# Optimization experiments

Hardware: AMD Instinct MI355X
Metric: run time of the kernel (lower is better)

Reference implementation:

```python
import jax, jax.numpy as jnp
import numpy as np

L, H, D, HS, DFF, V, B, T = 4, 16, 1024, 64, 5120, 32000, 2, 1024
EPS = 1e-5


def setup_inputs() -> dict:
    key = jax.random.key(0)
    ks = iter(jax.random.split(key, 40))
    def nrm(shape):
        return jax.random.normal(next(ks), shape, dtype=jnp.float32) * 0.02
    inp = {}
    inp['idx'] = jax.random.randint(next(ks), (B, T), 0, V)
    inp['tok_emb'] = nrm((V, D))
    inp['pos_emb'] = nrm((T, D))
    for s in ('u', 'm'):  # u = unmasked heads, m = masked (causal) heads
        inp['Wq_' + s] = nrm((L, H, D, HS)); inp['bq_' + s] = jnp.zeros((L, H, HS), jnp.float32)
        inp['Wk_' + s] = nrm((L, H, D, HS)); inp['bk_' + s] = jnp.zeros((L, H, HS), jnp.float32)
        inp['Wv_' + s] = nrm((L, H, D, HS)); inp['bv_' + s] = jnp.zeros((L, H, HS), jnp.float32)
        inp['Wp_' + s] = nrm((L, D, D));     inp['bp_' + s] = jnp.zeros((L, D), jnp.float32)
    inp['W1'] = nrm((L, D, DFF)); inp['b1'] = jnp.zeros((L, DFF), jnp.float32)
    inp['W2'] = nrm((L, DFF, D)); inp['b2'] = jnp.zeros((L, D), jnp.float32)
    ones = jnp.ones((L, D), jnp.float32); zer = jnp.zeros((L, D), jnp.float32)
    inp['lnf_g'] = ones; inp['lnf_b'] = zer     # LayerNorm inside FeedForward
    inp['n1_g'] = ones;  inp['n1_b'] = zer      # Block.norm1
    inp['n2_g'] = ones;  inp['n2_b'] = zer      # Block.norm2
    inp['nf_g'] = jnp.ones((D,), jnp.float32); inp['nf_b'] = jnp.zeros((D,), jnp.float32)
    inp['Wfin'] = nrm((D, V)); inp['bfin'] = jnp.zeros((V,), jnp.float32)
    return inp


def _ln(x, g, b):
    mu = jnp.mean(x, -1, keepdims=True)
    var = jnp.mean((x - mu) ** 2, -1, keepdims=True)
    return (x - mu) / jnp.sqrt(var + EPS) * g + b


def _attn(xn, Wq, bq, Wk, bk, Wv, bv, Wp, bp, causal):
    # xn: [B,T,D]; Wq/Wk/Wv: [H,D,HS] (all heads batched in one einsum)
    q = jnp.einsum('btd,hde->bhte', xn, Wq) + bq[:, None, :]
    k = jnp.einsum('btd,hde->bhte', xn, Wk) + bk[:, None, :]
    v = jnp.einsum('btd,hde->bhte', xn, Wv) + bv[:, None, :]
    w = jnp.einsum('bhte,bhse->bhts', q, k) * (HS ** -0.5)
    if causal:
        mask = jnp.tril(jnp.ones((w.shape[-2], w.shape[-1]), bool))
        w = jnp.where(mask, w, -jnp.inf)
    w = jax.nn.softmax(w, axis=-1)
    o = jnp.einsum('bhts,bhse->bhte', w, v)
    o = o.transpose(0, 2, 1, 3).reshape(xn.shape[0], xn.shape[1], -1)  # concat heads
    return o @ Wp + bp


def _ffn(x, W1, b1, W2, b2, g, b):
    h = jax.nn.leaky_relu(x @ W1 + b1, negative_slope=0.01)
    return _ln(h @ W2 + b2, g, b)


def reference(idx, tok_emb, pos_emb,
              Wq_u, bq_u, Wk_u, bk_u, Wv_u, bv_u, Wp_u, bp_u,
              Wq_m, bq_m, Wk_m, bk_m, Wv_m, bv_m, Wp_m, bp_m,
              W1, b1, W2, b2, lnf_g, lnf_b, n1_g, n1_b, n2_g, n2_b,
              nf_g, nf_b, Wfin, bfin):
    Tn = idx.shape[1]
    x = tok_emb[idx] + pos_emb[:Tn]
    for l in range(L):
        # exact quirky Block wiring from the original code
        x2 = x + _attn(_ln(x, n1_g[l], n1_b[l]), Wq_u[l], bq_u[l], Wk_u[l], bk_u[l],
                       Wv_u[l], bv_u[l], Wp_u[l], bp_u[l], False)
        x = x2 + _ln(_ffn(_ln(x2, n2_g[l], n2_b[l]), W1[l], b1[l], W2[l], b2[l],
                          lnf_g[l], lnf_b[l]), n1_g[l], n1_b[l])
        x2 = x + _attn(_ln(x, n1_g[l], n1_b[l]), Wq_m[l], bq_m[l], Wk_m[l], bk_m[l],
                       Wv_m[l], bv_m[l], Wp_m[l], bp_m[l], True)
        x = x2 + _ln(_ffn(_ln(x2, n2_g[l], n2_b[l]), W1[l], b1[l], W2[l], b2[l],
                          lnf_g[l], lnf_b[l]), n2_g[l], n2_b[l])
    x = _ln(x, nf_g, nf_b)
    return x @ Wfin + bfin  # logits [B,T,V]; targets=None path -> loss is None
```

## Files before the change

### kernel.cpp

```cpp
#include <hip/hip_runtime.h>
#include <hip/hip_bf16.h>
#include <math.h>

#define LNUM 4
#define H 16
#define D 1024
#define HS 64
#define DFF 5120
#define V 32000
#define BB 2
#define T 1024
#define M (BB*T)
#define EPS 1e-5f

typedef __attribute__((ext_vector_type(8))) short bf16x8;
typedef __attribute__((ext_vector_type(4))) float f32x4;

__device__ __forceinline__ void gload16(const void* g, void* l) {
    __builtin_amdgcn_global_load_lds(
        (const __attribute__((address_space(1))) void*)g,
        (__attribute__((address_space(3))) void*)l, 16, 0, 0);
}

__device__ __forceinline__ float wred_sum(float v) {
    #pragma unroll
    for (int off = 32; off; off >>= 1) v += __shfl_xor(v, off, 64);
    return v;
}

__global__ __launch_bounds__(256) void embed_ln_kernel(const int* __restrict__ idx,
        const float* __restrict__ tok, const float* __restrict__ pos,
        const float* __restrict__ g, const float* __restrict__ b,
        float* __restrict__ x, __hip_bfloat16* __restrict__ xn) {
    int w = threadIdx.x >> 6, lane = threadIdx.x & 63;
    int row = blockIdx.x * 4 + w;
    int t = row & (T - 1);
    int tok_id = idx[row];
    const float* tp = tok + (size_t)tok_id * D;
    const float* pp = pos + (size_t)t * D;
    float4 xv[4];
    float s = 0.f;
    #pragma unroll
    for (int c = 0; c < 4; ++c) {
        int j = c * 256 + lane * 4;
        float4 a = *(const float4*)&tp[j];
        float4 p = *(const float4*)&pp[j];
        a.x += p.x; a.y += p.y; a.z += p.z; a.w += p.w;
        *(float4*)&x[(size_t)row * D + j] = a;
        xv[c] = a;
        s += a.x + a.y + a.z + a.w;
    }
    float mu = wred_sum(s) * (1.0f / D);
    float vs = 0.f;
    #pragma unroll
    for (int c = 0; c < 4; ++c) {
        xv[c].x -= mu; xv[c].y -= mu; xv[c].z -= mu; xv[c].w -= mu;
        vs += xv[c].x*xv[c].x + xv[c].y*xv[c].y + xv[c].z*xv[c].z + xv[c].w*xv[c].w;
    }
    float rs = rsqrtf(wred_sum(vs) * (1.0f / D) + EPS);
    #pragma unroll
    for (int c = 0; c < 4; ++c) {
        int j = c * 256 + lane * 4;
        float4 gv = *(const float4*)&g[j];
        float4 bv = *(const float4*)&b[j];
        union { ushort4 u4; __hip_bfloat16 h[4]; } pk;
        pk.h[0] = __float2bfloat16(xv[c].x * rs * gv.x + bv.x);
        pk.h[1] = __float2bfloat16(xv[c].y * rs * gv.y + bv.y);
        pk.h[2] = __float2bfloat16(xv[c].z * rs * gv.z + bv.z);
        pk.h[3] = __float2bfloat16(xv[c].w * rs * gv.w + bv.w);
        *(ushort4*)&xn[(size_t)row * D + j] = pk.u4;
    }
}

__global__ __launch_bounds__(256) void ln_bf16_w4_kernel(const float* __restrict__ in,
        const float* __restrict__ g, const float* __restrict__ b,
        __hip_bfloat16* __restrict__ out) {
    int w = threadIdx.x >> 6, lane = threadIdx.x & 63;
    int row = blockIdx.x * 4 + w;
    const float* rp = in + (size_t)row * D;
    float4 xv[4];
    float s = 0.f;
    #pragma unroll
    for (int c = 0; c < 4; ++c) {
        xv[c] = *(const float4*)&rp[c * 256 + lane * 4];
        s += xv[c].x + xv[c].y + xv[c].z + xv[c].w;
    }
    float mu = wred_sum(s) * (1.0f / D);
    float vs = 0.f;
    #pragma unroll
    for (int c = 0; c < 4; ++c) {
        xv[c].x -= mu; xv[c].y -= mu; xv[c].z -= mu; xv[c].w -= mu;
        vs += xv[c].x*xv[c].x + xv[c].y*xv[c].y + xv[c].z*xv[c].z + xv[c].w*xv[c].w;
    }
    float rs = rsqrtf(wred_sum(vs) * (1.0f / D) + EPS);
    #pragma unroll
    for (int c = 0; c < 4; ++c) {
        int j = c * 256 + lane * 4;
        float4 gv = *(const float4*)&g[j];
        float4 bv = *(const float4*)&b[j];
        union { ushort4 u4; __hip_bfloat16 h[4]; } pk;
        pk.h[0] = __float2bfloat16(xv[c].x * rs * gv.x + bv.x);
        pk.h[1] = __float2bfloat16(xv[c].y * rs * gv.y + bv.y);
        pk.h[2] = __float2bfloat16(xv[c].z * rs * gv.z + bv.z);
        pk.h[3] = __float2bfloat16(xv[c].w * rs * gv.w + bv.w);
        *(ushort4*)&out[(size_t)row * D + j] = pk.u4;
    }
}

template<int NP>
__global__ __launch_bounds__(256) void ffn_tail_kernel(
        const float* __restrict__ part, const float* __restrict__ b2,
        const float* __restrict__ g1, const float* __restrict__ b1,
        const float* __restrict__ g2, const float* __restrict__ b2g,
        const float* __restrict__ res, float* __restrict__ xout,
        const float* __restrict__ gn, const float* __restrict__ bn,
        __hip_bfloat16* __restrict__ xnout) {
    const size_t MD = (size_t)M * D;
    int w = threadIdx.x >> 6, lane = threadIdx.x & 63;
    int row = blockIdx.x * 4 + w;
    size_t ro = (size_t)row * D;
    float4 f[4];
    float s = 0.f;
    #pragma unroll
    for (int c = 0; c < 4; ++c) {
        int j = c * 256 + lane * 4;
        float4 acc = *(const float4*)&b2[j];
        #pragma unroll
        for (int pI = 0; pI < NP; ++pI) {
            float4 pv = *(const float4*)&part[pI * MD + ro + j];
            acc.x += pv.x; acc.y += pv.y; acc.z += pv.z; acc.w += pv.w;
        }
        f[c] = acc;
        s += acc.x + acc.y + acc.z + acc.w;
    }
    float mu = wred_sum(s) * (1.0f / D);
    float vs = 0.f;
    #pragma unroll
    for (int c = 0; c < 4; ++c) {
        f[c].x -= mu; f[c].y -= mu; f[c].z -= mu; f[c].w -= mu;
        vs += f[c].x*f[c].x + f[c].y*f[c].y + f[c].z*f[c].z + f[c].w*f[c].w;
    }
    float rs = rsqrtf(wred_sum(vs) * (1.0f / D) + EPS);
    float s2 = 0.f;
    #pragma unroll
    for (int c = 0; c < 4; ++c) {
        int j = c * 256 + lane * 4;
        float4 gv = *(const float4*)&g1[j];
        float4 bv = *(const float4*)&b1[j];
        f[c].x = f[c].x * rs * gv.x + bv.x;
        f[c].y = f[c].y * rs * gv.y + bv.y;
        f[c].z = f[c].z * rs * gv.z + bv.z;
        f[c].w = f[c].w * rs * gv.w + bv.w;
        s2 += f[c].x + f[c].y + f[c].z + f[c].w;
    }
    float mu2 = wred_sum(s2) * (1.0f / D);
    float vs2 = 0.f;
    #pragma unroll
    for (int c = 0; c < 4; ++c) {
        f[c].x -= mu2; f[c].y -= mu2; f[c].z -= mu2; f[c].w -= mu2;
        vs2 += f[c].x*f[c].x + f[c].y*f[c].y + f[c].z*f[c].z + f[c].w*f[c].w;
    }
    float rs2 = rsqrtf(wred_sum(vs2) * (1.0f / D) + EPS);
    float s3 = 0.f;
    #pragma unroll
    for (int c = 0; c < 4; ++c) {
        int j = c * 256 + lane * 4;
        float4 gv = *(const float4*)&g2[j];
        float4 bv = *(const float4*)&b2g[j];
        float4 rv = *(const float4*)&res[ro + j];
        f[c].x = rv.x + f[c].x * rs2 * gv.x + bv.x;
        f[c].y = rv.y + f[c].y * rs2 * gv.y + bv.y;
        f[c].z = rv.z + f[c].z * rs2 * gv.z + bv.z;
        f[c].w = rv.w + f[c].w * rs2 * gv.w + bv.w;
        *(float4*)&xout[ro + j] = f[c];
        s3 += f[c].x + f[c].y + f[c].z + f[c].w;
    }
    float mu3 = wred_sum(s3) * (1.0f / D);
    float vs3 = 0.f;
    #pragma unroll
    for (int c = 0; c < 4; ++c) {
        f[c].x -= mu3; f[c].y -= mu3; f[c].z -= mu3; f[c].w -= mu3;
        vs3 += f[c].x*f[c].x + f[c].y*f[c].y + f[c].z*f[c].z + f[c].w*f[c].w;
    }
    float rs3 = rsqrtf(wred_sum(vs3) * (1.0f / D) + EPS);
    #pragma unroll
    for (int c = 0; c < 4; ++c) {
        int j = c * 256 + lane * 4;
        float4 gv = *(const float4*)&gn[j];
        float4 bv = *(const float4*)&bn[j];
        union { ushort4 u4; __hip_bfloat16 h[4]; } pk;
        pk.h[0] = __float2bfloat16(f[c].x * rs3 * gv.x + bv.x);
        pk.h[1] = __float2bfloat16(f[c].y * rs3 * gv.y + bv.y);
        pk.h[2] = __float2bfloat16(f[c].z * rs3 * gv.z + bv.z);
        pk.h[3] = __float2bfloat16(f[c].w * rs3 * gv.w + bv.w);
        *(ushort4*)&xnout[ro + j] = pk.u4;
    }
}

__global__ __launch_bounds__(256) void transpose_bf16_kernel(
        const float* __restrict__ in, __hip_bfloat16* __restrict__ out,
        int R, int C) {
    __shared__ float t[32][33];
    int tx = threadIdx.x & 31, ty = threadIdx.x >> 5;
    int c0 = blockIdx.x * 32, r0 = blockIdx.y * 32;
    #pragma unroll
    for (int i = 0; i < 4; ++i)
        t[ty + i * 8][tx] = in[(size_t)(r0 + ty + i * 8) * C + c0 + tx];
    __syncthreads();
    #pragma unroll
    for (int i = 0; i < 4; ++i)
        out[(size_t)(c0 + ty + i * 8) * R + r0 + tx] = __float2bfloat16(t[tx][ty + i * 8]);
}

__global__ __launch_bounds__(256) void trans_qkvp_kernel(
        const float* __restrict__ Wq, const float* __restrict__ Wk,
        const float* __restrict__ Wv, const float* __restrict__ Wp,
        short* __restrict__ qkvT, short* __restrict__ WpT) {
    __shared__ float t[32][33];
    int tx = threadIdx.x & 31, ty = threadIdx.x >> 5;
    int z = blockIdx.z;
    const float* in;
    __hip_bfloat16* out;
    int inC, outC;
    int r0 = blockIdx.y * 32, c0;
    if (z < 3) {
        int c0g = blockIdx.x * 32;
        int h = c0g >> 6;
        c0 = c0g & 63;
        in = (z == 0 ? Wq : z == 1 ? Wk : Wv) + (size_t)h * D * HS;
        out = (__hip_bfloat16*)qkvT + ((size_t)z * H + h) * HS * D;
        inC = HS; outC = D;
    } else {
        c0 = blockIdx.x * 32;
        in = Wp; out = (__hip_bfloat16*)WpT;
        inC = D; outC = D;
    }
    #pragma unroll
    for (int i = 0; i < 4; ++i)
        t[ty + i * 8][tx] = in[(size_t)(r0 + ty + i * 8) * inC + c0 + tx];
    __syncthreads();
    #pragma unroll
    for (int i = 0; i < 4; ++i)
        out[(size_t)(c0 + ty + i * 8) * outC + r0 + tx] = __float2bfloat16(t[tx][ty + i * 8]);
}

__global__ __launch_bounds__(256) void trans_w12_kernel(
        const float* __restrict__ W1, const float* __restrict__ W2,
        short* __restrict__ W1T, short* __restrict__ W2T) {
    __shared__ float t[32][33];
    int tx = threadIdx.x & 31, ty = threadIdx.x >> 5;
    int z = blockIdx.z;
    const float* in; __hip_bfloat16* out;
    int inC, outC, r0, c0;
    if (z == 0) { in = W1; out = (__hip_bfloat16*)W1T; inC = DFF; outC = D;
                  r0 = blockIdx.y * 32; c0 = blockIdx.x * 32; }
    else        { in = W2; out = (__hip_bfloat16*)W2T; inC = D; outC = DFF;
                  r0 = blockIdx.x * 32; c0 = blockIdx.y * 32; }
    #pragma unroll
    for (int i = 0; i < 4; ++i)
        t[ty + i * 8][tx] = in[(size_t)(r0 + ty + i * 8) * inC + c0 + tx];
    __syncthreads();
    #pragma unroll
    for (int i = 0; i < 4; ++i)
        out[(size_t)(c0 + ty + i * 8) * outC + r0 + tx] = __float2bfloat16(t[tx][ty + i * 8]);
}

__global__ __launch_bounds__(256) void transpose_v_kernel(const short* __restrict__ in,
        short* __restrict__ out) {
    __shared__ short t[32][33];
    int z = blockIdx.z;
    in  += (size_t)z * T * HS;
    out += (size_t)z * HS * T;
    int tx = threadIdx.x & 31, ty = threadIdx.x >> 5;
    int c0 = blockIdx.x * 32, r0 = blockIdx.y * 32;
    #pragma unroll
    for (int i = 0; i < 4; ++i)
        t[ty + i * 8][tx] = in[(size_t)(r0 + ty + i * 8) * HS + c0 + tx];
    __syncthreads();
    #pragma unroll
    for (int i = 0; i < 4; ++i)
        out[(size_t)(c0 + ty + i * 8) * T + r0 + tx] = t[tx][ty + i * 8];
}

template<int EPI>
__global__ __launch_bounds__(512, 2) void mm256_kernel(
        const short* __restrict__ A, const short* __restrict__ BT,
        const float* __restrict__ bias0, float* __restrict__ C0,
        __hip_bfloat16* __restrict__ Cbf, int N, int Kloop, int lda) {
    __shared__ __align__(16) char LA[2][2][256 * 64];
    __shared__ __align__(16) char LB[2][2][256 * 64];
    int tid = threadIdx.x;
    int lane = tid & 63, wid = tid >> 6;
    int wr = wid >> 2, wc = wid & 3;
    int l15 = lane & 15, l16 = lane >> 4;

    int nwg = gridDim.x;
    int bid = blockIdx.x;
    int q = nwg >> 3, r = nwg & 7;
    int xcd = bid & 7, loc = bid >> 3;
    int wg = (xcd < r ? xcd * (q + 1) : r * (q + 1) + (xcd - r) * q) + loc;
    int m0 = (wg & 7) * 256;
    int n0 = (wg >> 3) * 256;

    const size_t lda2 = (size_t)lda * 2;
    const char* Agc = (const char*)A + (size_t)m0 * lda2;
    const char* Bgc = (const char*)BT + (size_t)n0 * lda2;

    f32x4 acc[8][4] = {};
    bf16x8 af[8], bfr[4];

    auto stA = [&](int buf, int kh, int kt) {
        #pragma unroll
        for (int i = 0; i < 2; ++i) {
            int o = i * 8192 + tid * 16;
            int row = o >> 6, col = o & 63;
            gload16(Agc + (size_t)row * lda2 + kt * 128 + kh * 64 +
                    (col ^ (((row >> 1) & 3) << 4)), LA[buf][kh] + o);
        }
    };
    auto stB = [&](int buf, int kh, int kt) {
        #pragma unroll
        for (int i = 0; i < 2; ++i) {
            int o = i * 8192 + tid * 16;
            int row = o >> 6, col = o & 63;
            gload16(Bgc + (size_t)row * lda2 + kt * 128 + kh * 64 +
                    (col ^ (((row >> 1) & 3) << 4)), LB[buf][kh] + o);
        }
    };
    auto rdA = [&](int buf, int kk) {
        #pragma unroll
        for (int mf = 0; mf < 8; ++mf) {
            int row = wr * 128 + mf * 16 + l15;
            af[mf] = *(const bf16x8*)(LA[buf][kk] + row * 64 +
                      ((l16 * 16) ^ (((row >> 1) & 3) << 4)));
        }
    };
    auto rdB4 = [&](int buf, int kk) {
        #pragma unroll
        for (int nf = 0; nf < 4; ++nf) {
            int row = wc * 64 + nf * 16 + l15;
            bfr[nf] = *(const bf16x8*)(LB[buf][kk] + row * 64 +
                       ((l16 * 16) ^ (((row >> 1) & 3) << 4)));
        }
    };
    auto mfma32 = [&]() {
        __builtin_amdgcn_s_setprio(1);
        #pragma unroll
        for (int mf = 0; mf < 8; ++mf)
            #pragma unroll
            for (int nf = 0; nf < 4; ++nf)
                acc[mf][nf] = __builtin_amdgcn_mfma_f32_16x16x32_bf16(
                    af[mf], bfr[nf], acc[mf][nf], 0, 0, 0);
        __builtin_amdgcn_s_setprio(0);
    };

    const int NT = Kloop / 64;
    stA(0, 0, 0); stB(0, 0, 0); stA(0, 1, 0); stB(0, 1, 0);
    stA(1, 0, 1); stB(1, 0, 1);
    asm volatile("s_waitcnt vmcnt(4)" ::: "memory");
    __builtin_amdgcn_sched_barrier(0);
    __builtin_amdgcn_s_barrier();
    __builtin_amdgcn_sched_barrier(0);

    for (int t = 0; t < NT; ++t) {
        int buf = t & 1;
        rdA(buf, 0); rdB4(buf, 0);
        if (t + 1 < NT) { stA(buf ^ 1, 1, t + 1); stB(buf ^ 1, 1, t + 1); }
        mfma32();
        __builtin_amdgcn_sched_barrier(0);
        __builtin_amdgcn_s_barrier();
        __builtin_amdgcn_sched_barrier(0);
        rdA(buf, 1); rdB4(buf, 1);
        if (t + 2 < NT) { stA(buf, 0, t + 2); stB(buf, 0, t + 2); }
        mfma32();
        if (t + 2 < NT) { asm volatile("s_waitcnt vmcnt(4)" ::: "memory"); }
        else            { asm volatile("s_waitcnt vmcnt(0)" ::: "memory"); }
        __builtin_amdgcn_sched_barrier(0);
        __builtin_amdgcn_s_barrier();
        __builtin_amdgcn_sched_barrier(0);
    }

    #pragma unroll
    for (int mf = 0; mf < 8; ++mf) {
        #pragma unroll
        for (int nf = 0; nf < 4; ++nf) {
            int col = n0 + wc * 64 + nf * 16 + l15;
            float bv = bias0[col];
            #pragma unroll
            for (int rr = 0; rr < 4; ++rr) {
                int row = m0 + wr * 128 + mf * 16 + l16 * 4 + rr;
                float v = acc[mf][nf][rr] + bv;
                if (EPI == 0) {
                    C0[(size_t)row * N + col] = v;
                } else {
                    v = v > 0.f ? v : 0.01f * v;
                    Cbf[(size_t)row * N + col] = __float2bfloat16(v);
                }
            }
        }
    }
}

template<int BM, int EPI>
__global__ __launch_bounds__(256) void mm_bf16_kernel(
        const short* __restrict__ A, const short* __restrict__ BT,
        const float* __restrict__ bias0, const float* __restrict__ bias1,
        const float* __restrict__ bias2, const float* __restrict__ res,
        float* __restrict__ C0, float* __restrict__ C1, float* __restrict__ C2,
        __hip_bfloat16* __restrict__ Cbf, int N, int Kloop, int lda) {
    constexpr int MI = BM / 32;
    __shared__ __align__(16) char As[2][BM * 128];
    __shared__ __align__(16) char Bs[2][128 * 128];
    int nwg = gridDim.x * gridDim.y;
    int bid = blockIdx.y * gridDim.x + blockIdx.x;
    int bx = blockIdx.x, by = blockIdx.y;
    if (!(nwg & 7)) {
        int s = (bid & 7) * (nwg >> 3) + (bid >> 3);
        bx = s % gridDim.x; by = s / gridDim.x;
    }
    int tid = threadIdx.x;
    int lane = tid & 63, wid = tid >> 6;
    int wr = wid >> 1, wc = wid & 1;
    int l15 = lane & 15, l16 = lane >> 4;
    int m0 = bx * BM, n0 = by * 128;
    f32x4 acc[MI][4] = {};

    const size_t lda2 = (size_t)lda * 2;
    const char* Agc = (const char*)A + (size_t)m0 * lda2 + (size_t)blockIdx.z * Kloop * 2;
    const char* Bgc = (const char*)BT + (size_t)n0 * lda2 + (size_t)blockIdx.z * Kloop * 2;

    auto stage = [&](int buf, int kbyte) {
        #pragma unroll
        for (int i = 0; i < BM / 32; ++i) {
            int o = i * 4096 + tid * 16;
            int row = o >> 7, col = o & 127;
            gload16(Agc + (size_t)row * lda2 + kbyte + (col ^ ((row & 7) << 4)),
                    As[buf] + o);
        }
        #pragma unroll
        for (int i = 0; i < 4; ++i) {
            int o = i * 4096 + tid * 16;
            int row = o >> 7, col = o & 127;
            gload16(Bgc + (size_t)row * lda2 + kbyte + (col ^ ((row & 7) << 4)),
                    Bs[buf] + o);
        }
    };
    auto compute = [&](int buf) {
        #pragma unroll
        for (int kk = 0; kk < 2; ++kk) {
            bf16x8 af[MI], bfr[4];
            #pragma unroll
            for (int mi = 0; mi < MI; ++mi) {
                int row = wr * (BM / 2) + mi * 16 + l15;
                af[mi] = *(const bf16x8*)(As[buf] + row * 128 +
                          ((kk * 64 + l16 * 16) ^ ((row & 7) << 4)));
            }
            #pragma unroll
            for (int ni = 0; ni < 4; ++ni) {
                int row = wc * 64 + ni * 16 + l15;
                bfr[ni] = *(const bf16x8*)(Bs[buf] + row * 128 +
                          ((kk * 64 + l16 * 16) ^ ((row & 7) << 4)));
            }
            __builtin_amdgcn_s_setprio(1);
            #pragma unroll
            for (int mi = 0; mi < MI; ++mi)
                #pragma unroll
                for (int ni = 0; ni < 4; ++ni)
                    acc[mi][ni] = __builtin_amdgcn_mfma_f32_16x16x32_bf16(
                        af[mi], bfr[ni], acc[mi][ni], 0, 0, 0);
            __builtin_amdgcn_s_setprio(0);
        }
    };

    const int NT = Kloop / 64;
    stage(0, 0);
    stage(1, 128);
    for (int t = 0; t < NT; ++t) {
        if (t < NT - 1) {
            if constexpr (BM == 128) asm volatile("s_waitcnt vmcnt(8)" ::: "memory");
            else                     asm volatile("s_waitcnt vmcnt(6)" ::: "memory");
        } else {
            asm volatile("s_waitcnt vmcnt(0)" ::: "memory");
        }
        __builtin_amdgcn_sched_barrier(0);
        __builtin_amdgcn_s_barrier();
        __builtin_amdgcn_sched_barrier(0);
        compute(t & 1);
        __builtin_amdgcn_s_barrier();
        __builtin_amdgcn_sched_barrier(0);
        if (t + 2 < NT) stage(t & 1, (t + 2) * 128);
    }

    int rbase = m0 + wr * (BM / 2) + l16 * 4;
    int cbase = n0 + wc * 64 + l15;
    size_t zoff = (EPI == 4) ? (size_t)blockIdx.z * M * N : 0;
    #pragma unroll
    for (int mi = 0; mi < MI; ++mi) {
        #pragma unroll
        for (int ni = 0; ni < 4; ++ni) {
            int col = cbase + ni * 16;
            float bv = 0.f;
            if (EPI == 3) {
                int z = col >> 10, nn = col & 1023;
                bv = (z == 0 ? bias0 : z == 1 ? bias1 : bias2)[nn];
            } else if (EPI != 4) bv = bias0[col];
            #pragma unroll
            for (int r = 0; r < 4; ++r) {
                int row = rbase + mi * 16 + r;
                float v = acc[mi][ni][r] + bv;
                if (EPI == 0) {
                    C0[(size_t)row * N + col] = v;
                } else if (EPI == 1) {
                    C0[(size_t)row * N + col] = v + res[(size_t)row * N + col];
                } else if (EPI == 2) {
                    v = v > 0.f ? v : 0.01f * v;
                    Cbf[(size_t)row * N + col] = __float2bfloat16(v);
                } else if (EPI == 4) {
                    C0[zoff + (size_t)row * N + col] = v;
                } else {
                    int z = col >> 10;
                    int hh = (col >> 6) & 15, e = col & 63;
                    int b = row >> 10, t2 = row & (T - 1);
                    __hip_bfloat16* dst = (__hip_bfloat16*)(z == 0 ? C0 : (z == 1 ? C1 : C2));
                    dst[(((size_t)(b * H + hh)) * T + t2) * HS + e] = __float2bfloat16(v);
                }
            }
        }
    }
}

template<int CAUSAL>
__global__ __launch_bounds__(256) void attn_mfma_kernel(
        const short* __restrict__ q, const short* __restrict__ k,
        const short* __restrict__ vt, __hip_bfloat16* __restrict__ att) {
    __shared__ __align__(16) short Ks[128 * 64];
    __shared__ __align__(16) short Vs[64 * 128];
    __shared__ __align__(16) short Ps[4][16 * 128];
    int bh = blockIdx.y;
    int bI = bh >> 4, h = bh & 15;
    int tix = blockIdx.x;
    if (CAUSAL) tix = (tix & 1) ? (15 - (tix >> 1)) : (tix >> 1);
    int t0 = tix * 64;
    int tid = threadIdx.x;
    int lane = tid & 63, w = tid >> 6;
    int l15 = lane & 15, l16 = lane >> 4;

    const short* Qg = q + ((size_t)bh * T + t0 + w * 16 + l15) * HS + l16 * 8;
    bf16x8 qf0 = *(const bf16x8*)Qg;
    bf16x8 qf1 = *(const bf16x8*)(Qg + 32);

    const char* Kg = (const char*)(k + (size_t)bh * T * HS);
    const char* Vg = (const char*)(vt + (size_t)bh * HS * T);

    float m_run[4] = {-1e30f, -1e30f, -1e30f, -1e30f};
    float l_run[4] = {0.f, 0.f, 0.f, 0.f};
    f32x4 acc_o[4] = {};
    char* Pw = (char*)Ps[w];
    int pswz = l15 << 4;

    int n_tiles = CAUSAL ? (t0 / 128 + 1) : (T / 128);
    for (int it = 0; it < n_tiles; ++it) {
        int s0 = it * 128;
        __syncthreads();
        #pragma unroll
        for (int i = 0; i < 4; ++i) {
            int o = i * 4096 + tid * 16;
            int row = o >> 7, bir = o & 127;
            gload16(Kg + (size_t)(s0 + row) * 128 + (bir ^ ((row & 7) << 4)),
                    (char*)Ks + o);
        }
        #pragma unroll
        for (int i = 0; i < 4; ++i) {
            int o = i * 4096 + tid * 16;
            int row = o >> 8, bb = o & 255;
            gload16(Vg + (size_t)row * 2048 + s0 * 2 + (bb ^ ((row & 15) << 4)),
                    (char*)Vs + o);
        }
        __syncthreads();

        f32x4 acc_s[8] = {};
        __builtin_amdgcn_s_setprio(1);
        #pragma unroll
        for (int c = 0; c < 8; ++c) {
            int row = c * 16 + l15;
            const char* kb_ = (const char*)Ks + row * 128;
            int swz = (row & 7) << 4;
            bf16x8 kf0 = *(const bf16x8*)(kb_ + ((l16 * 16) ^ swz));
            bf16x8 kf1 = *(const bf16x8*)(kb_ + ((64 + l16 * 16) ^ swz));
            acc_s[c] = __builtin_amdgcn_mfma_f32_16x16x32_bf16(qf0, kf0, acc_s[c], 0, 0, 0);
            acc_s[c] = __builtin_amdgcn_mfma_f32_16x16x32_bf16(qf1, kf1, acc_s[c], 0, 0, 0);
        }
        __builtin_amdgcn_s_setprio(0);

        bool domask = CAUSAL && (it == n_tiles - 1);
        #pragma unroll
        for (int r = 0; r < 4; ++r) {
            float sc[8];
            #pragma unroll
            for (int c = 0; c < 8; ++c) {
                float s = acc_s[c][r];
                if (domask && (s0 + c * 16 + l15) > (t0 + w * 16 + l16 * 4 + r)) s = -1e30f;
                sc[c] = s;
            }
            float tm = fmaxf(fmaxf(fmaxf(sc[0], sc[1]), fmaxf(sc[2], sc[3])),
                             fmaxf(fmaxf(sc[4], sc[5]), fmaxf(sc[6], sc[7])));
            tm = fmaxf(tm, __shfl_xor(tm, 1, 16));
            tm = fmaxf(tm, __shfl_xor(tm, 2, 16));
            tm = fmaxf(tm, __shfl_xor(tm, 4, 16));
            tm = fmaxf(tm, __shfl_xor(tm, 8, 16));
            float mn = fmaxf(m_run[r], tm);
            int prow = l16 * 4 + r;
            int pswzr = prow << 4;
            float ls = 0.f;
            #pragma unroll
            for (int c = 0; c < 8; ++c) {
                float pv = __expf(0.125f * (sc[c] - mn));
                int pbyte = prow * 256 + (((c * 16 + l15) * 2) ^ pswzr);
                *(__hip_bfloat16*)(Pw + pbyte) = __float2bfloat16(pv);
                ls += pv;
            }
            ls += __shfl_xor(ls, 1, 16);
            ls += __shfl_xor(ls, 2, 16);
            ls += __shfl_xor(ls, 4, 16);
            ls += __shfl_xor(ls, 8, 16);
            float alpha = __expf(0.125f * (m_run[r] - mn));
            l_run[r] = l_run[r] * alpha + ls;
            m_run[r] = mn;
            acc_o[0][r] *= alpha; acc_o[1][r] *= alpha;
            acc_o[2][r] *= alpha; acc_o[3][r] *= alpha;
        }

        const char* Pb = Pw + l15 * 256;
        bf16x8 pa[4];
        #pragma unroll
        for (int t = 0; t < 4; ++t)
            pa[t] = *(const bf16x8*)(Pb + ((t * 64 + l16 * 16) ^ pswz));
        __builtin_amdgcn_s_setprio(1);
        #pragma unroll
        for (int ni = 0; ni < 4; ++ni) {
            int row = ni * 16 + l15;
            const char* vb_ = (const char*)Vs + row * 256;
            int swz = (row & 15) << 4;
            #pragma unroll
            for (int t = 0; t < 4; ++t) {
                bf16x8 vf = *(const bf16x8*)(vb_ + ((t * 64 + l16 * 16) ^ swz));
                acc_o[ni] = __builtin_amdgcn_mfma_f32_16x16x32_bf16(pa[t], vf, acc_o[ni], 0, 0, 0);
            }
        }
        __builtin_amdgcn_s_setprio(0);
    }

    float inv[4];
    #pragma unroll
    for (int r = 0; r < 4; ++r) inv[r] = 1.0f / l_run[r];
    #pragma unroll
    for (int ni = 0; ni < 4; ++ni) {
        #pragma unroll
        for (int r = 0; r < 4; ++r) {
            size_t orow = ((size_t)(bI * T) + t0 + w * 16 + l16 * 4 + r) * D
                        + h * HS + ni * 16 + l15;
            att[orow] = __float2bfloat16(acc_o[ni][r] * inv[r]);
        }
    }
}

extern "C" void kernel_launch(void* const* d_in, const int* in_sizes, int n_in,
                              void* d_out, int out_size, void* d_ws, size_t ws_size,
                              hipStream_t stream) {
    const int*   idx     = (const int*)d_in[0];
    const float* tok_emb = (const float*)d_in[1];
    const float* pos_emb = (const float*)d_in[2];
    const float* Wq_u = (const float*)d_in[3],  *bq_u = (const float*)d_in[4];
    const float* Wk_u = (const float*)d_in[5],  *bk_u = (const float*)d_in[6];
    const float* Wv_u = (const float*)d_in[7],  *bv_u = (const float*)d_in[8];
    const float* Wp_u = (const float*)d_in[9],  *bp_u = (const float*)d_in[10];
    const float* Wq_m = (const float*)d_in[11], *bq_m = (const float*)d_in[12];
    const float* Wk_m = (const float*)d_in[13], *bk_m = (const float*)d_in[14];
    const float* Wv_m = (const float*)d_in[15], *bv_m = (const float*)d_in[16];
    const float* Wp_m = (const float*)d_in[17], *bp_m = (const float*)d_in[18];
    const float* W1   = (const float*)d_in[19], *b1   = (const float*)d_in[20];
    const float* W2   = (const float*)d_in[21], *b2   = (const float*)d_in[22];
    const float* lnf_g = (const float*)d_in[23], *lnf_b = (const float*)d_in[24];
    const float* n1_g  = (const float*)d_in[25], *n1_b  = (const float*)d_in[26];
    const float* n2_g  = (const float*)d_in[27], *n2_b  = (const float*)d_in[28];
    const float* nf_g  = (const float*)d_in[29], *nf_b  = (const float*)d_in[30];
    const float* Wfin  = (const float*)d_in[31], *bfin  = (const float*)d_in[32];
    float* out = (float*)d_out;

    char* p = (char*)d_ws;
    auto alloc = [&](size_t bytes) { char* r = p; p += (bytes + 255) & ~255ull; return r; };
    float* x    = (float*)alloc((size_t)M * D * 4);
    float* x2   = (float*)alloc((size_t)M * D * 4);
    float* w2p  = (float*)alloc((size_t)4 * M * D * 4);
    short* qbf  = (short*)alloc((size_t)M * D * 2);
    short* kbf  = (short*)alloc((size_t)M * D * 2);
    short* vbf  = (short*)alloc((size_t)M * D * 2);
    short* vtb  = (short*)alloc((size_t)M * D * 2);
    short* xnb  = (short*)alloc((size_t)M * D * 2);
    short* attb = (short*)alloc((size_t)M * D * 2);
    short* hb   = (short*)alloc((size_t)M * DFF * 2);
    short* WqkvT= (short*)alloc((size_t)3 * 1024 * 1024 * 2);
    short* WpT  = (short*)alloc((size_t)1024 * 1024 * 2);
    short* W1T  = (short*)alloc((size_t)D * DFF * 2);
    short* W2T  = (short*)alloc((size_t)DFF * D * 2);
    short* WfT  = (short*)alloc((size_t)D * V * 2);

    embed_ln_kernel<<<M / 4, 256, 0, stream>>>(idx, tok_emb, pos_emb,
        n1_g, n1_b, x, (__hip_bfloat16*)xnb);
    transpose_bf16_kernel<<<dim3(V / 32, D / 32), 256, 0, stream>>>(
        Wfin, (__hip_bfloat16*)WfT, D, V);

    for (int l = 0; l < LNUM; ++l) {
        const float *n1g = n1_g + l * D, *n1b = n1_b + l * D;
        const float *n2g = n2_g + l * D, *n2b = n2_b + l * D;
        const float *lfg = lnf_g + l * D, *lfb = lnf_b + l * D;
        const float *W1l = W1 + (size_t)l * D * DFF, *b1l = b1 + l * DFF;
        const float *W2l = W2 + (size_t)l * DFF * D, *b2l = b2 + l * D;
        trans_w12_kernel<<<dim3(160, 32, 2), 256, 0, stream>>>(
            W1l, W2l, W1T, W2T);
        for (int half = 0; half < 2; ++half) {
            const float *Wq_, *bq_, *Wk_, *bk_, *Wv_, *bv_, *Wp_, *bp_;
            if (half == 0) { Wq_ = Wq_u; bq_ = bq_u; Wk_ = Wk_u; bk_ = bk_u;
                             Wv_ = Wv_u; bv_ = bv_u; Wp_ = Wp_u; bp_ = bp_u; }
            else           { Wq_ = Wq_m; bq_ = bq_m; Wk_ = Wk_m; bk_ = bk_m;
                             Wv_ = Wv_m; bv_ = bv_m; Wp_ = Wp_m; bp_ = bp_m; }
            Wq_ += (size_t)l * H * D * HS;  bq_ += l * H * HS;
            Wk_ += (size_t)l * H * D * HS;  bk_ += l * H * HS;
            Wv_ += (size_t)l * H * D * HS;  bv_ += l * H * HS;
            Wp_ += (size_t)l * D * D;       bp_ += l * D;

            trans_qkvp_kernel<<<dim3(32, 32, 4), 256, 0, stream>>>(
                Wq_, Wk_, Wv_, Wp_, WqkvT, WpT);

            mm_bf16_kernel<128, 3><<<dim3(M / 128, 3072 / 128), 256, 0, stream>>>(
                xnb, WqkvT, bq_, bk_, bv_, nullptr,
                (float*)qbf, (float*)kbf, (float*)vbf, nullptr, 3072, D, D);
            transpose_v_kernel<<<dim3(HS / 32, T / 32, BB * H), 256, 0, stream>>>(vbf, vtb);
            if (half == 0)
                attn_mfma_kernel<0><<<dim3(T / 64, BB * H), 256, 0, stream>>>(
                    qbf, kbf, vtb, (__hip_bfloat16*)attb);
            else
                attn_mfma_kernel<1><<<dim3(T / 64, BB * H), 256, 0, stream>>>(
                    qbf, kbf, vtb, (__hip_bfloat16*)attb);
            mm_bf16_kernel<64, 1><<<dim3(M / 64, D / 128), 256, 0, stream>>>(
                attb, WpT, bp_, nullptr, nullptr, x, x2, nullptr, nullptr, nullptr, D, D, D);
            ln_bf16_w4_kernel<<<M / 4, 256, 0, stream>>>(x2, n2g, n2b, (__hip_bfloat16*)xnb);
            mm256_kernel<2><<<(M / 256) * (DFF / 256), 512, 0, stream>>>(
                xnb, W1T, b1l, nullptr, (__hip_bfloat16*)hb, DFF, D, D);
            mm_bf16_kernel<128, 4><<<dim3(M / 128, D / 128, 4), 256, 0, stream>>>(
                hb, W2T, nullptr, nullptr, nullptr, nullptr, w2p, nullptr, nullptr,
                nullptr, D, DFF / 4, DFF);
            const float* og = half ? n2g : n1g;
            const float* ob = half ? n2b : n1b;
            const float* gn; const float* bn;
            if (half == 0)      { gn = n1g; bn = n1b; }
            else if (l < LNUM-1){ gn = n1_g + (l+1)*D; bn = n1_b + (l+1)*D; }
            else                { gn = nf_g; bn = nf_b; }
            ffn_tail_kernel<4><<<M / 4, 256, 0, stream>>>(
                w2p, b2l, lfg, lfb, og, ob, x2, x, gn, bn, (__hip_bfloat16*)xnb);
        }
    }
    mm256_kernel<0><<<(M / 256) * (V / 256), 512, 0, stream>>>(
        xnb, WfT, bfin, out, nullptr, V, D, D);
}
```

Baseline: 1.519 ms.

## Halve GEMM LDS staging to a single K-half per buffer and raise occupancy

Restructures the 256x256 bf16 GEMM main loop. Each stage now holds one 32-wide K slice per double-buffer slot instead of two 64-byte halves, which halves shared memory per block. The interleaved read/issue/MFMA schedule becomes a simpler wait, compute, then prefetch loop with two barriers per step. The launch bound is raised to 4 blocks per CU to gain occupancy. The risk is that capping registers that hard, with 128 accumulator floats per thread, may force spills. Shorter K steps also mean more barriers and less overlap of loads with compute.

```diff
diff --git a/kernel.cpp b/kernel.cpp
--- a/kernel.cpp
+++ b/kernel.cpp
@@ -283,12 +283,12 @@
 }
 
 template<int EPI>
-__global__ __launch_bounds__(512, 2) void mm256_kernel(
+__global__ __launch_bounds__(512, 4) void mm256_kernel(
         const short* __restrict__ A, const short* __restrict__ BT,
         const float* __restrict__ bias0, float* __restrict__ C0,
         __hip_bfloat16* __restrict__ Cbf, int N, int Kloop, int lda) {
-    __shared__ __align__(16) char LA[2][2][256 * 64];
-    __shared__ __align__(16) char LB[2][2][256 * 64];
+    __shared__ __align__(16) char LA[2][256 * 64];
+    __shared__ __align__(16) char LB[2][256 * 64];
     int tid = threadIdx.x;
     int lane = tid & 63, wid = tid >> 6;
     int wr = wid >> 2, wc = wid & 3;
@@ -307,43 +307,37 @@
     const char* Bgc = (const char*)BT + (size_t)n0 * lda2;
 
     f32x4 acc[8][4] = {};
-    bf16x8 af[8], bfr[4];
-
-    auto stA = [&](int buf, int kh, int kt) {
+
+    auto stage = [&](int buf, int kt) {
         #pragma unroll
         for (int i = 0; i < 2; ++i) {
             int o = i * 8192 + tid * 16;
             int row = o >> 6, col = o & 63;
-            gload16(Agc + (size_t)row * lda2 + kt * 128 + kh * 64 +
-                    (col ^ (((row >> 1) & 3) << 4)), LA[buf][kh] + o);
-        }
-    };
-    auto stB = [&](int buf, int kh, int kt) {
+            int sw = col ^ ((((row >> 1) & 3)) << 4);
+            gload16(Agc + (size_t)row * lda2 + kt * 64 + sw, LA[buf] + o);
+        }
         #pragma unroll
         for (int i = 0; i < 2; ++i) {
             int o = i * 8192 + tid * 16;
             int row = o >> 6, col = o & 63;
-            gload16(Bgc + (size_t)row * lda2 + kt * 128 + kh * 64 +
-                    (col ^ (((row >> 1) & 3) << 4)), LB[buf][kh] + o);
+            int sw = col ^ ((((row >> 1) & 3)) << 4);
+            gload16(Bgc + (size_t)row * lda2 + kt * 64 + sw, LB[buf] + o);
         }
     };
-    auto rdA = [&](int buf, int kk) {
+    auto compute = [&](int buf) {
+        bf16x8 af[8], bfr[4];
         #pragma unroll
         for (int mf = 0; mf < 8; ++mf) {
             int row = wr * 128 + mf * 16 + l15;
-            af[mf] = *(const bf16x8*)(LA[buf][kk] + row * 64 +
+            af[mf] = *(const bf16x8*)(LA[buf] + row * 64 +
                       ((l16 * 16) ^ (((row >> 1) & 3) << 4)));
         }
-    };
-    auto rdB4 = [&](int buf, int kk) {
         #pragma unroll
         for (int nf = 0; nf < 4; ++nf) {
             int row = wc * 64 + nf * 16 + l15;
-            bfr[nf] = *(const bf16x8*)(LB[buf][kk] + row * 64 +
+            bfr[nf] = *(const bf16x8*)(LB[buf] + row * 64 +
                        ((l16 * 16) ^ (((row >> 1) & 3) << 4)));
         }
-    };
-    auto mfma32 = [&]() {
         __builtin_amdgcn_s_setprio(1);
         #pragma unroll
         for (int mf = 0; mf < 8; ++mf)
@@ -354,30 +348,19 @@
         __builtin_amdgcn_s_setprio(0);
     };
 
-    const int NT = Kloop / 64;
-    stA(0, 0, 0); stB(0, 0, 0); stA(0, 1, 0); stB(0, 1, 0);
-    stA(1, 0, 1); stB(1, 0, 1);
-    asm volatile("s_waitcnt vmcnt(4)" ::: "memory");
-    __builtin_amdgcn_sched_barrier(0);
-    __builtin_amdgcn_s_barrier();
-    __builtin_amdgcn_sched_barrier(0);
-
+    const int NT = Kloop / 32;
+    stage(0, 0);
+    stage(1, 1);
     for (int t = 0; t < NT; ++t) {
-        int buf = t & 1;
-        rdA(buf, 0); rdB4(buf, 0);
-        if (t + 1 < NT) { stA(buf ^ 1, 1, t + 1); stB(buf ^ 1, 1, t + 1); }
-        mfma32();
-        __builtin_amdgcn_sched_barrier(0);
-        __builtin_amdgcn_s_barrier();
-        __builtin_amdgcn_sched_barrier(0);
-        rdA(buf, 1); rdB4(buf, 1);
-        if (t + 2 < NT) { stA(buf, 0, t + 2); stB(buf, 0, t + 2); }
-        mfma32();
-        if (t + 2 < NT) { asm volatile("s_waitcnt vmcnt(4)" ::: "memory"); }
+        if (t < NT - 1) { asm volatile("s_waitcnt vmcnt(4)" ::: "memory"); }
         else            { asm volatile("s_waitcnt vmcnt(0)" ::: "memory"); }
         __builtin_amdgcn_sched_barrier(0);
         __builtin_amdgcn_s_barrier();
         __builtin_amdgcn_sched_barrier(0);
+        compute(t & 1);
+        __builtin_amdgcn_s_barrier();
+        __builtin_amdgcn_sched_barrier(0);
+        if (t + 2 < NT) stage(t & 1, t + 2);
     }
 
     #pragma unroll
```

Result: slower. 4.413 ms (+190.5%).

## Double-buffer K/V tiles in attention kernel to overlap loads with MFMA

Applied to the files above, without the earlier changes.

The attention kernel now keeps two LDS buffers for K and V and issues the async global-to-LDS loads for the next tile before computing on the current one. It waits with a partial vmcnt so only the current tile's loads must have landed, which is meant to hide global-load latency behind the QK and PV MFMA work. The cost is doubled K/V LDS usage, which may lower occupancy. Attention is only a small part of the full model, so the end-to-end effect is limited.

```diff
diff --git a/kernel.cpp b/kernel.cpp
--- a/kernel.cpp
+++ b/kernel.cpp
@@ -533,8 +533,8 @@
 __global__ __launch_bounds__(256) void attn_mfma_kernel(
         const short* __restrict__ q, const short* __restrict__ k,
         const short* __restrict__ vt, __hip_bfloat16* __restrict__ att) {
-    __shared__ __align__(16) short Ks[128 * 64];
-    __shared__ __align__(16) short Vs[64 * 128];
+    __shared__ __align__(16) short Ks[2][128 * 64];
+    __shared__ __align__(16) short Vs[2][64 * 128];
     __shared__ __align__(16) short Ps[4][16 * 128];
     int bh = blockIdx.y;
     int bI = bh >> 4, h = bh & 15;
@@ -558,32 +558,44 @@
     char* Pw = (char*)Ps[w];
     int pswz = l15 << 4;
 
-    int n_tiles = CAUSAL ? (t0 / 128 + 1) : (T / 128);
-    for (int it = 0; it < n_tiles; ++it) {
-        int s0 = it * 128;
-        __syncthreads();
+    auto stageKV = [&](int buf, int s0) {
         #pragma unroll
         for (int i = 0; i < 4; ++i) {
             int o = i * 4096 + tid * 16;
             int row = o >> 7, bir = o & 127;
             gload16(Kg + (size_t)(s0 + row) * 128 + (bir ^ ((row & 7) << 4)),
-                    (char*)Ks + o);
+                    (char*)Ks[buf] + o);
         }
         #pragma unroll
         for (int i = 0; i < 4; ++i) {
             int o = i * 4096 + tid * 16;
             int row = o >> 8, bb = o & 255;
             gload16(Vg + (size_t)row * 2048 + s0 * 2 + (bb ^ ((row & 15) << 4)),
-                    (char*)Vs + o);
-        }
-        __syncthreads();
+                    (char*)Vs[buf] + o);
+        }
+    };
+
+    int n_tiles = CAUSAL ? (t0 / 128 + 1) : (T / 128);
+    stageKV(0, 0);
+    for (int it = 0; it < n_tiles; ++it) {
+        int buf = it & 1;
+        int s0 = it * 128;
+        if (it + 1 < n_tiles) {
+            stageKV(buf ^ 1, (it + 1) * 128);
+            asm volatile("s_waitcnt vmcnt(8)" ::: "memory");
+        } else {
+            asm volatile("s_waitcnt vmcnt(0)" ::: "memory");
+        }
+        __builtin_amdgcn_sched_barrier(0);
+        __builtin_amdgcn_s_barrier();
+        __builtin_amdgcn_sched_barrier(0);
 
         f32x4 acc_s[8] = {};
         __builtin_amdgcn_s_setprio(1);
         #pragma unroll
         for (int c = 0; c < 8; ++c) {
             int row = c * 16 + l15;
-            const char* kb_ = (const char*)Ks + row * 128;
+            const char* kb_ = (const char*)Ks[buf] + row * 128;
             int swz = (row & 7) << 4;
             bf16x8 kf0 = *(const bf16x8*)(kb_ + ((l16 * 16) ^ swz));
             bf16x8 kf1 = *(const bf16x8*)(kb_ + ((64 + l16 * 16) ^ swz));
@@ -633,21 +645,23 @@
         const char* Pb = Pw + l15 * 256;
         bf16x8 pa[4];
         #pragma unroll
-        for (int t = 0; t < 4; ++t)
-            pa[t] = *(const bf16x8*)(Pb + ((t * 64 + l16 * 16) ^ pswz));
+        for (int tt = 0; tt < 4; ++tt)
+            pa[tt] = *(const bf16x8*)(Pb + ((tt * 64 + l16 * 16) ^ pswz));
         __builtin_amdgcn_s_setprio(1);
         #pragma unroll
         for (int ni = 0; ni < 4; ++ni) {
             int row = ni * 16 + l15;
-            const char* vb_ = (const char*)Vs + row * 256;
+            const char* vb_ = (const char*)Vs[buf] + row * 256;
             int swz = (row & 15) << 4;
             #pragma unroll
-            for (int t = 0; t < 4; ++t) {
-                bf16x8 vf = *(const bf16x8*)(vb_ + ((t * 64 + l16 * 16) ^ swz));
-                acc_o[ni] = __builtin_amdgcn_mfma_f32_16x16x32_bf16(pa[t], vf, acc_o[ni], 0, 0, 0);
+            for (int tt = 0; tt < 4; ++tt) {
+                bf16x8 vf = *(const bf16x8*)(vb_ + ((tt * 64 + l16 * 16) ^ swz));
+                acc_o[ni] = __builtin_amdgcn_mfma_f32_16x16x32_bf16(pa[tt], vf, acc_o[ni], 0, 0, 0);
             }
         }
         __builtin_amdgcn_s_setprio(0);
+        __builtin_amdgcn_s_barrier();
+        __builtin_amdgcn_sched_barrier(0);
     }
 
     float inv[4];
```

Measured after the change: 1.526 ms. About the same (+0.5%).
